# Kernel optimization log

Measured on AMD Instinct MI355X. Metric: run time of the kernel, lower is better.

## Reference

```python
import jax, jax.numpy as jnp
import numpy as np

TF = 512  # text_features
VF = 512  # video_features


def setup_inputs() -> dict:
    key = jax.random.key(0)
    k1, k2, k3 = jax.random.split(key, 3)
    text = jax.random.normal(k1, (4, 32, TF), dtype=jnp.float32)
    video = jax.random.normal(k2, (4, 64, 196, VF), dtype=jnp.float32)
    # nn.Linear(text_features + video_features, 1): weight (1, TF+VF), bias (1,)
    w = jax.random.normal(k3, (TF + VF,), dtype=jnp.float32) * (1.0 / np.sqrt(TF + VF))
    b = jnp.zeros((1,), dtype=jnp.float32)
    return {"text": text, "video": video, "w": w, "b": b}


def reference(text, video, w, b):
    # Split the 1-output linear over the concat into text-only and video-only
    # projections: Linear(cat([t, v])) = t @ wt + v @ wv + b  (exact algebra).
    tf = text.shape[-1]
    wt, wv = w[:tf], w[tf:]
    score_t = jnp.einsum('btf,f->bt', text, wt) + b[0]        # (B, St)
    score_v = jnp.einsum('bvhf,f->bvh', video, wv)            # (B, Sv, HW)
    scores = score_t[:, :, None, None] + score_v[:, None]     # (B, St, Sv, HW)
    B, St, Sv, HW = scores.shape
    # softmax over the flattened (Sv*HW) dim, per (b, st)
    weights = jax.nn.softmax(scores.reshape(B, St, Sv * HW), axis=-1)
    weights = weights.reshape(B, St, Sv, HW)
    # fused[b,st,sv,f] = sum_hw weights[b,st,sv,hw] * video[b,sv,hw,f]
    fused = jnp.einsum('bsvh,bvhf->bsvf', weights, video)
    return fused
```

## Files before the change

### kernel.cpp

```cpp
#include <hip/hip_runtime.h>

#define TF 512
#define VF 512
#define BB 4
#define ST 32
#define SV 64
#define HW 196
#define NBV (BB * SV)
#define NSEG 4
#define SEGH (HW / NSEG)


__global__ __launch_bounds__(256) void score_acc_kernel(const float4* __restrict__ video,
                                                        const float* __restrict__ w,
                                                        float4* __restrict__ Gpart,
                                                        float* __restrict__ dpart) {
    int bv   = blockIdx.x >> 2;
    int seg  = blockIdx.x & 3;
    int tid  = threadIdx.x;
    int wave = tid >> 6;
    int lane = tid & 63;

    const float4* wv4 = (const float4*)(w + TF);
    float4 w0 = wv4[lane];
    float4 w1 = wv4[lane + 64];

    const float4* vbase = video + ((size_t)bv * HW + seg * SEGH) * (VF / 4);

    float4 acc0 = make_float4(0.f, 0.f, 0.f, 0.f);
    float4 acc1 = make_float4(0.f, 0.f, 0.f, 0.f);
    float  esum = 0.f;

    #pragma unroll 2
    for (int hl = wave; hl < SEGH; hl += 4) {
        const float4* row = vbase + hl * (VF / 4);
        float4 x0 = row[lane];
        float4 x1 = row[lane + 64];
        float s = x0.x * w0.x + x0.y * w0.y + x0.z * w0.z + x0.w * w0.w
                + x1.x * w1.x + x1.y * w1.y + x1.z * w1.z + x1.w * w1.w;
        #pragma unroll
        for (int off = 32; off > 0; off >>= 1)
            s += __shfl_xor(s, off, 64);
        float e = __expf(s);
        esum += e;
        acc0.x = fmaf(e, x0.x, acc0.x);
        acc0.y = fmaf(e, x0.y, acc0.y);
        acc0.z = fmaf(e, x0.z, acc0.z);
        acc0.w = fmaf(e, x0.w, acc0.w);
        acc1.x = fmaf(e, x1.x, acc1.x);
        acc1.y = fmaf(e, x1.y, acc1.y);
        acc1.z = fmaf(e, x1.z, acc1.z);
        acc1.w = fmaf(e, x1.w, acc1.w);
    }

    __shared__ float4 sacc[4][VF / 4];
    __shared__ float  sd[4];
    sacc[wave][lane]      = acc0;
    sacc[wave][lane + 64] = acc1;
    if (lane == 0) sd[wave] = esum;
    __syncthreads();

    int c = tid & 127, half = tid >> 7;
    float4 a  = sacc[half * 2][c];
    float4 bq = sacc[half * 2 + 1][c];
    float4 t  = make_float4(a.x + bq.x, a.y + bq.y, a.z + bq.z, a.w + bq.w);
    sacc[half * 2][c] = t;
    __syncthreads();
    if (half == 0) {
        float4 u = sacc[2][c];
        Gpart[((size_t)seg * NBV + bv) * (VF / 4) + c] =
            make_float4(t.x + u.x, t.y + u.y, t.z + u.z, t.w + u.w);
    }
    if (tid == 0) dpart[blockIdx.x] = sd[0] + sd[1] + sd[2] + sd[3];
}

__global__ __launch_bounds__(256) void out_kernel(const float4* __restrict__ Gpart,
                                                  const float* __restrict__ dpart,
                                                  float4* __restrict__ out) {
    int bv  = blockIdx.x >> 2;
    int q   = blockIdx.x & 3;
    int b   = bv >> 6;
    int v   = bv & 63;
    int tid = threadIdx.x;

    __shared__ float red[4];

    float val = dpart[b * 256 + tid];
    #pragma unroll
    for (int off = 32; off > 0; off >>= 1) val += __shfl_xor(val, off, 64);
    if ((tid & 63) == 0) red[tid >> 6] = val;

    int c = tid & 127, half = tid >> 7;
    float4 g0 = Gpart[((size_t)0 * NBV + bv) * (VF / 4) + c];
    float4 g1 = Gpart[((size_t)1 * NBV + bv) * (VF / 4) + c];
    float4 g2 = Gpart[((size_t)2 * NBV + bv) * (VF / 4) + c];
    float4 g3 = Gpart[((size_t)3 * NBV + bv) * (VF / 4) + c];
    __syncthreads();

    float inv = 1.0f / (red[0] + red[1] + red[2] + red[3]);
    float4 res = make_float4((g0.x + g1.x + g2.x + g3.x) * inv,
                             (g0.y + g1.y + g2.y + g3.y) * inv,
                             (g0.z + g1.z + g2.z + g3.z) * inv,
                             (g0.w + g1.w + g2.w + g3.w) * inv);

    #pragma unroll
    for (int k = 0; k < 4; k++) {
        int s = q * 8 + half * 4 + k;
        out[(((size_t)(b * ST + s)) * SV + v) * (VF / 4) + c] = res;
    }
}

extern "C" void kernel_launch(void* const* d_in, const int* in_sizes, int n_in,
                              void* d_out, int out_size, void* d_ws, size_t ws_size,
                              hipStream_t stream) {
    const float* video = (const float*)d_in[1];
    const float* w     = (const float*)d_in[2];
    float4* Gpart = (float4*)d_ws;
    float*  dpart = (float*)((char*)d_ws + (size_t)NSEG * NBV * (VF / 4) * sizeof(float4));

    score_acc_kernel<<<NBV * NSEG, 256, 0, stream>>>((const float4*)video, w,
                                                     Gpart, dpart);
    out_kernel<<<NBV * NSEG, 256, 0, stream>>>(Gpart, dpart, (float4*)d_out);
}
```

Before: 166.3 us.

## Fuse score and output kernels with a global atomic grid barrier

Merges the score/accumulate kernel and the output kernel into one launch, using an atomic counter spin barrier so every block waits for all partial sums before writing its output slice. It is meant to remove the second kernel launch and the gap between the two kernels. In exchange it adds a memset launch, relies on all 1024 blocks being co-resident (launch bounds hint of 4 blocks per SM), and has a spin timeout that could yield wrong results if residency fails.

```diff
diff --git a/kernel.cpp b/kernel.cpp
--- a/kernel.cpp
+++ b/kernel.cpp
@@ -9,12 +9,14 @@
 #define NBV (BB * SV)
 #define NSEG 4
 #define SEGH (HW / NSEG)
+#define NBLK (NBV * NSEG)
 
 
-__global__ __launch_bounds__(256) void score_acc_kernel(const float4* __restrict__ video,
-                                                        const float* __restrict__ w,
-                                                        float4* __restrict__ Gpart,
-                                                        float* __restrict__ dpart) {
+__global__ __launch_bounds__(256, 4) void fused_kernel(
+        const float4* __restrict__ video, const float* __restrict__ w,
+        float4* __restrict__ Gpart, float* __restrict__ dpart,
+        unsigned int* __restrict__ counter, float4* __restrict__ out) {
+
     int bv   = blockIdx.x >> 2;
     int seg  = blockIdx.x & 3;
     int tid  = threadIdx.x;
@@ -55,6 +57,8 @@
 
     __shared__ float4 sacc[4][VF / 4];
     __shared__ float  sd[4];
+    __shared__ float  red[4];
+
     sacc[wave][lane]      = acc0;
     sacc[wave][lane + 64] = acc1;
     if (lane == 0) sd[wave] = esum;
@@ -72,25 +76,28 @@
             make_float4(t.x + u.x, t.y + u.y, t.z + u.z, t.w + u.w);
     }
     if (tid == 0) dpart[blockIdx.x] = sd[0] + sd[1] + sd[2] + sd[3];
-}
 
-__global__ __launch_bounds__(256) void out_kernel(const float4* __restrict__ Gpart,
-                                                  const float* __restrict__ dpart,
-                                                  float4* __restrict__ out) {
-    int bv  = blockIdx.x >> 2;
-    int q   = blockIdx.x & 3;
-    int b   = bv >> 6;
-    int v   = bv & 63;
-    int tid = threadIdx.x;
+    __syncthreads();
+    if (tid == 0) {
+        __threadfence();
+        atomicAdd(counter, 1u);
+        unsigned spins = 0;
+        while (__hip_atomic_load(counter, __ATOMIC_RELAXED, __HIP_MEMORY_SCOPE_AGENT) < NBLK) {
+            __builtin_amdgcn_s_sleep(8);
+            if (++spins > (1u << 20)) break;
+        }
+    }
+    __syncthreads();
+    __threadfence();
 
-    __shared__ float red[4];
+    int b = bv >> 6;
+    int v = bv & 63;
 
     float val = dpart[b * 256 + tid];
     #pragma unroll
     for (int off = 32; off > 0; off >>= 1) val += __shfl_xor(val, off, 64);
     if ((tid & 63) == 0) red[tid >> 6] = val;
 
-    int c = tid & 127, half = tid >> 7;
     float4 g0 = Gpart[((size_t)0 * NBV + bv) * (VF / 4) + c];
     float4 g1 = Gpart[((size_t)1 * NBV + bv) * (VF / 4) + c];
     float4 g2 = Gpart[((size_t)2 * NBV + bv) * (VF / 4) + c];
@@ -105,7 +112,7 @@
 
     #pragma unroll
     for (int k = 0; k < 4; k++) {
-        int s = q * 8 + half * 4 + k;
+        int s = seg * 8 + half * 4 + k;
         out[(((size_t)(b * ST + s)) * SV + v) * (VF / 4) + c] = res;
     }
 }
@@ -115,10 +122,16 @@
                               hipStream_t stream) {
     const float* video = (const float*)d_in[1];
     const float* w     = (const float*)d_in[2];
+
+    size_t gpart_bytes = (size_t)NSEG * NBV * (VF / 4) * sizeof(float4);
+    size_t dpart_bytes = (size_t)NBLK * sizeof(float);
     float4* Gpart = (float4*)d_ws;
-    float*  dpart = (float*)((char*)d_ws + (size_t)NSEG * NBV * (VF / 4) * sizeof(float4));
+    float*  dpart = (float*)((char*)d_ws + gpart_bytes);
+    unsigned int* counter = (unsigned int*)((char*)d_ws + gpart_bytes + dpart_bytes + 128);
 
-    score_acc_kernel<<<NBV * NSEG, 256, 0, stream>>>((const float4*)video, w,
-                                                     Gpart, dpart);
-    out_kernel<<<NBV * NSEG, 256, 0, stream>>>(Gpart, dpart, (float4*)d_out);
+    hipMemsetAsync(counter, 0, sizeof(unsigned int), stream);
+
+    fused_kernel<<<NBLK, 256, 0, stream>>>((const float4*)video, w,
+                                           Gpart, dpart, counter,
+                                           (float4*)d_out);
 }
```

Measured after the change: 304.0 us. +82.8%, slower.
